# Optimization experiments

Hardware: AMD Instinct MI355X
Metric: run time of the kernel (lower is better)

The kernel has to match this reference:

```python
import jax, jax.numpy as jnp
import numpy as np

NUM_NODES = 100000
EMBED_DIM = 256
NUM_EDGES = 16384
TOTAL = 524288  # total flattened hyperedge membership entries


def setup_inputs() -> dict:
    key = jax.random.key(0)
    k1, k2, k3 = jax.random.split(key, 3)
    node_embeddings = jax.random.normal(k1, (NUM_NODES, EMBED_DIM), dtype=jnp.float32)
    node_indices = jax.random.randint(k2, (TOTAL,), 0, NUM_NODES, dtype=jnp.int64)
    segment_ids = jnp.sort(jax.random.randint(k3, (TOTAL,), 0, NUM_EDGES, dtype=jnp.int64))
    return {"node_embeddings": node_embeddings, "node_indices": node_indices, "segment_ids": segment_ids}


def reference(node_embeddings, node_indices, segment_ids):
    # Gather member-node embeddings: [TOTAL, D]
    gathered = node_embeddings[node_indices]
    # Segmented sum over hyperedges: [NUM_EDGES, D]
    seg_sum = jax.ops.segment_sum(gathered, segment_ids, num_segments=NUM_EDGES)
    # Per-hyperedge member counts for the mean; guard empty segments.
    counts = jax.ops.segment_sum(jnp.ones((gathered.shape[0],), dtype=gathered.dtype),
                                 segment_ids, num_segments=NUM_EDGES)
    counts = jnp.maximum(counts, 1.0)
    return seg_sum / counts[:, None]
```

## Files before the change

kernel.cpp:

```cpp
#include <hip/hip_runtime.h>


#define EMBED_DIM 256
#define NUM_EDGES 16384
#define TOTAL_MEM 524288

__global__ __launch_bounds__(256) void seg_bounds_kernel(
    const int* __restrict__ seg_ids,
    int*       __restrict__ seg_start)
{
    const int i = blockIdx.x * blockDim.x + threadIdx.x;
    if (i >= TOTAL_MEM) return;
    const int cur  = seg_ids[i];
    const int prev = (i == 0) ? -1 : seg_ids[i - 1];
    for (int s = prev + 1; s <= cur; ++s) seg_start[s] = i;
    if (i == TOTAL_MEM - 1) {
        for (int s = cur + 1; s <= NUM_EDGES; ++s) seg_start[s] = TOTAL_MEM;
    }
}

__global__ __launch_bounds__(256) void hyperedge_agg_kernel(
    const float* __restrict__ emb,
    const int*   __restrict__ node_idx,
    const int*   __restrict__ seg_start,
    float*       __restrict__ out)
{
    const int wave = threadIdx.x >> 6;
    const int lane = threadIdx.x & 63;
    const int seg  = blockIdx.x * 4 + wave;
    if (seg >= NUM_EDGES) return;

    const int start = seg_start[seg];
    const int end   = seg_start[seg + 1];

    float4 acc = make_float4(0.f, 0.f, 0.f, 0.f);

    int i = start;
    while (i < end) {
        const int batch = min(end - i, 64);
        const int my = (lane < batch) ? node_idx[i + lane] : 0;
        const int nGroups = (batch + 7) >> 3;

        float4 v0[8], v1[8];

        int m0 = min(batch, 8);
        #pragma unroll
        for (int t = 0; t < 8; ++t)
            if (t < m0) {
                const int n = __shfl(my, t);
                v0[t] = ((const float4*)(emb + (size_t)n * EMBED_DIM))[lane];
            }

        for (int g = 1; g < nGroups; ++g) {
            const int j  = g << 3;
            const int m1 = min(batch - j, 8);
            #pragma unroll
            for (int t = 0; t < 8; ++t)
                if (t < m1) {
                    const int n = __shfl(my, j + t);
                    v1[t] = ((const float4*)(emb + (size_t)n * EMBED_DIM))[lane];
                }
            #pragma unroll
            for (int t = 0; t < 8; ++t) {
                acc.x += v0[t].x; acc.y += v0[t].y;
                acc.z += v0[t].z; acc.w += v0[t].w;
            }
            #pragma unroll
            for (int t = 0; t < 8; ++t) v0[t] = v1[t];
            m0 = m1;
        }

        #pragma unroll
        for (int t = 0; t < 8; ++t)
            if (t < m0) {
                acc.x += v0[t].x; acc.y += v0[t].y;
                acc.z += v0[t].z; acc.w += v0[t].w;
            }

        i += batch;
    }

    const float cnt = (end > start) ? (float)(end - start) : 1.0f;
    acc.x /= cnt; acc.y /= cnt; acc.z /= cnt; acc.w /= cnt;

    ((float4*)(out + (size_t)seg * EMBED_DIM))[lane] = acc;
}

__global__ __launch_bounds__(256) void hyperedge_agg_bsearch_kernel(
    const float* __restrict__ emb,
    const int*   __restrict__ node_idx,
    const int*   __restrict__ seg_ids,
    float*       __restrict__ out)
{
    const int wave = threadIdx.x >> 6;
    const int lane = threadIdx.x & 63;
    const int seg  = blockIdx.x * 4 + wave;
    if (seg >= NUM_EDGES) return;

    int lo = 0, hi = TOTAL_MEM;
    while (lo < hi) {
        int mid = (lo + hi) >> 1;
        if (seg_ids[mid] < seg) lo = mid + 1; else hi = mid;
    }
    const int start = lo;
    hi = TOTAL_MEM;
    while (lo < hi) {
        int mid = (lo + hi) >> 1;
        if (seg_ids[mid] < seg + 1) lo = mid + 1; else hi = mid;
    }
    const int end = lo;

    float4 acc = make_float4(0.f, 0.f, 0.f, 0.f);
    for (int i = start; i < end; ++i) {
        const int n = node_idx[i];
        float4 v = ((const float4*)(emb + (size_t)n * EMBED_DIM))[lane];
        acc.x += v.x; acc.y += v.y; acc.z += v.z; acc.w += v.w;
    }
    const float cnt = (end > start) ? (float)(end - start) : 1.0f;
    acc.x /= cnt; acc.y /= cnt; acc.z /= cnt; acc.w /= cnt;
    ((float4*)(out + (size_t)seg * EMBED_DIM))[lane] = acc;
}

extern "C" void kernel_launch(void* const* d_in, const int* in_sizes, int n_in,
                              void* d_out, int out_size, void* d_ws, size_t ws_size,
                              hipStream_t stream) {
    const float* emb      = (const float*)d_in[0];
    const int*   node_idx = (const int*)d_in[1];
    const int*   seg_ids  = (const int*)d_in[2];
    float*       out      = (float*)d_out;

    const size_t bounds_bytes = (size_t)(NUM_EDGES + 1) * sizeof(int);
    if (ws_size >= bounds_bytes) {
        int* seg_start = (int*)d_ws;
        seg_bounds_kernel<<<(TOTAL_MEM + 255) / 256, 256, 0, stream>>>(seg_ids, seg_start);
        hyperedge_agg_kernel<<<NUM_EDGES / 4, 256, 0, stream>>>(emb, node_idx, seg_start, out);
    } else {
        hyperedge_agg_bsearch_kernel<<<NUM_EDGES / 4, 256, 0, stream>>>(emb, node_idx, seg_ids, out);
    }
}
```

Before: 205.7 us.

## Split each hyperedge across four waves with LDS reduction

Each hyperedge now gets a whole block of four waves instead of one wave. Member rows are strided across the waves, and each wave keeps up to 16 gathers in flight with a two-stage register prefetch. The per-wave partial sums are combined through shared memory after a block barrier. This aims to raise memory-level parallelism and shorten the per-segment serial gather chain, at the cost of four times as many blocks, a __syncthreads, and an LDS reduction per segment.

```diff
diff --git a/kernel.cpp b/kernel.cpp
--- a/kernel.cpp
+++ b/kernel.cpp
@@ -25,65 +25,69 @@
     const int*   __restrict__ seg_start,
     float*       __restrict__ out)
 {
+    __shared__ float4 partial[4][64];
+
     const int wave = threadIdx.x >> 6;
     const int lane = threadIdx.x & 63;
-    const int seg  = blockIdx.x * 4 + wave;
-    if (seg >= NUM_EDGES) return;
+    const int seg  = blockIdx.x;
 
     const int start = seg_start[seg];
     const int end   = seg_start[seg + 1];
 
     float4 acc = make_float4(0.f, 0.f, 0.f, 0.f);
 
-    int i = start;
-    while (i < end) {
-        const int batch = min(end - i, 64);
-        const int my = (lane < batch) ? node_idx[i + lane] : 0;
-        const int nGroups = (batch + 7) >> 3;
+    for (int base = start; base < end; base += 64) {
+        const int batch = min(end - base, 64);
+        const int my = (lane < batch) ? node_idx[base + lane] : 0;
+        const int nMine = (batch > wave) ? ((batch - wave + 3) >> 2) : 0;
 
-        float4 v0[8], v1[8];
-
-        int m0 = min(batch, 8);
-        #pragma unroll
-        for (int t = 0; t < 8; ++t)
-            if (t < m0) {
-                const int n = __shfl(my, t);
-                v0[t] = ((const float4*)(emb + (size_t)n * EMBED_DIM))[lane];
-            }
-
-        for (int g = 1; g < nGroups; ++g) {
-            const int j  = g << 3;
-            const int m1 = min(batch - j, 8);
-            #pragma unroll
-            for (int t = 0; t < 8; ++t)
-                if (t < m1) {
-                    const int n = __shfl(my, j + t);
-                    v1[t] = ((const float4*)(emb + (size_t)n * EMBED_DIM))[lane];
-                }
-            #pragma unroll
-            for (int t = 0; t < 8; ++t) {
-                acc.x += v0[t].x; acc.y += v0[t].y;
-                acc.z += v0[t].z; acc.w += v0[t].w;
-            }
-            #pragma unroll
-            for (int t = 0; t < 8; ++t) v0[t] = v1[t];
-            m0 = m1;
-        }
+        float4 v[8];
+        const int m0 = min(nMine, 8);
 
         #pragma unroll
         for (int t = 0; t < 8; ++t)
             if (t < m0) {
-                acc.x += v0[t].x; acc.y += v0[t].y;
-                acc.z += v0[t].z; acc.w += v0[t].w;
+                const int n = __shfl(my, wave + (t << 2));
+                v[t] = ((const float4*)(emb + (size_t)n * EMBED_DIM))[lane];
             }
 
-        i += batch;
+        #pragma unroll
+        for (int t = 0; t < 8; ++t) {
+            if (t < m0) {
+                const float4 u = v[t];
+                const int t2 = t + 8;
+                if (t2 < nMine) {
+                    const int n = __shfl(my, wave + (t2 << 2));
+                    v[t] = ((const float4*)(emb + (size_t)n * EMBED_DIM))[lane];
+                }
+                acc.x += u.x; acc.y += u.y; acc.z += u.z; acc.w += u.w;
+            }
+        }
+        #pragma unroll
+        for (int t = 0; t < 8; ++t)
+            if (t + 8 < nMine) {
+                acc.x += v[t].x; acc.y += v[t].y;
+                acc.z += v[t].z; acc.w += v[t].w;
+            }
     }
 
-    const float cnt = (end > start) ? (float)(end - start) : 1.0f;
-    acc.x /= cnt; acc.y /= cnt; acc.z /= cnt; acc.w /= cnt;
+    partial[wave][lane] = acc;
+    __syncthreads();
 
-    ((float4*)(out + (size_t)seg * EMBED_DIM))[lane] = acc;
+    if (wave == 0) {
+        const float4 a = partial[0][lane];
+        const float4 b = partial[1][lane];
+        const float4 c = partial[2][lane];
+        const float4 d = partial[3][lane];
+        float4 s;
+        s.x = (a.x + b.x) + (c.x + d.x);
+        s.y = (a.y + b.y) + (c.y + d.y);
+        s.z = (a.z + b.z) + (c.z + d.z);
+        s.w = (a.w + b.w) + (c.w + d.w);
+        const float cnt = (end > start) ? (float)(end - start) : 1.0f;
+        s.x /= cnt; s.y /= cnt; s.z /= cnt; s.w /= cnt;
+        ((float4*)(out + (size_t)seg * EMBED_DIM))[lane] = s;
+    }
 }
 
 __global__ __launch_bounds__(256) void hyperedge_agg_bsearch_kernel(
@@ -133,7 +137,7 @@
     if (ws_size >= bounds_bytes) {
         int* seg_start = (int*)d_ws;
         seg_bounds_kernel<<<(TOTAL_MEM + 255) / 256, 256, 0, stream>>>(seg_ids, seg_start);
-        hyperedge_agg_kernel<<<NUM_EDGES / 4, 256, 0, stream>>>(emb, node_idx, seg_start, out);
+        hyperedge_agg_kernel<<<NUM_EDGES, 256, 0, stream>>>(emb, node_idx, seg_start, out);
     } else {
         hyperedge_agg_bsearch_kernel<<<NUM_EDGES / 4, 256, 0, stream>>>(emb, node_idx, seg_ids, out);
     }
```

Result: no change. 203.9 us (-0.9%).
